# Optimization experiments

Hardware: AMD Instinct MI355X
Metric: run time of the kernel (lower is better)

## Reference

```python
import jax, jax.numpy as jnp
import numpy as np

N_NODES, N_EDGES = 50000, 200000
DN, DE, DG = 256, 256, 128

def setup_inputs() -> dict:
    key = jax.random.key(0)
    ks = jax.random.split(key, 8)
    s = lambda d: 1.0 / np.sqrt(d)
    return {
        "nodes": jax.random.normal(ks[0], (N_NODES, DN), jnp.float32),
        "edges": jax.random.normal(ks[1], (N_EDGES, DE), jnp.float32),
        "globals_": jax.random.normal(ks[2], (DG,), jnp.float32),
        "senders": jax.random.randint(ks[3], (N_EDGES,), 0, N_NODES, jnp.int32),
        "receivers": jax.random.randint(ks[4], (N_EDGES,), 0, N_NODES, jnp.int32),
        "We": jax.random.normal(ks[5], (DE + 2 * DN + DG, DE), jnp.float32) * s(DE + 2 * DN + DG),
        "be": jnp.zeros((DE,), jnp.float32),
        "Wn": jax.random.normal(ks[6], (DE + DN + DG, DN), jnp.float32) * s(DE + DN + DG),
        "bn": jnp.zeros((DN,), jnp.float32),
        "Wg": jax.random.normal(ks[7], (DE + DN + DG, DG), jnp.float32) * s(DE + DN + DG),
        "bg": jnp.zeros((DG,), jnp.float32),
    }

def reference(nodes, edges, globals_, senders, receivers, We, be, Wn, bn, Wg, bg):
    E, N = edges.shape[0], nodes.shape[0]
    # --- edge processor: phi_e([e, v_s, v_r, u]) ---
    edge_in = jnp.concatenate(
        [edges, nodes[senders], nodes[receivers],
         jnp.broadcast_to(globals_, (E, globals_.shape[0]))], axis=-1)  # [E, 896]
    new_edges = jax.nn.relu(edge_in @ We + be)  # [E, DE]
    # --- node processor: phi_v([sum_incoming_e, v, u]) ---
    agg_e = jax.ops.segment_sum(new_edges, receivers, num_segments=N)  # [N, DE]
    node_in = jnp.concatenate(
        [agg_e, nodes, jnp.broadcast_to(globals_, (N, globals_.shape[0]))], axis=-1)
    new_nodes = jax.nn.relu(node_in @ Wn + bn)  # [N, DN]
    # --- global processor: phi_u([sum_e, sum_v, u]) ---
    global_in = jnp.concatenate(
        [new_edges.sum(axis=0), new_nodes.sum(axis=0), globals_], axis=-1)
    new_globals = jax.nn.relu(global_in @ Wg + bg)  # [DG]
    return new_edges, new_nodes, new_globals
```

## Files before the change

kernel.cpp:

```cpp
#include <hip/hip_runtime.h>

#define E_CNT 200000
#define N_CNT 50000

typedef __attribute__((ext_vector_type(8))) unsigned short ushort8;
typedef __attribute__((ext_vector_type(4))) unsigned short us4;
typedef __attribute__((ext_vector_type(4))) float f32x4;
typedef __bf16 bf16x8 __attribute__((ext_vector_type(8)));

static __device__ __forceinline__ unsigned short f2bf(float f) {
  unsigned int u = __builtin_bit_cast(unsigned int, f);
  u += 0x7FFFu + ((u >> 16) & 1u);
  return (unsigned short)(u >> 16);
}
static __device__ __forceinline__ float bf2f(unsigned short u) {
  unsigned int x = ((unsigned int)u) << 16;
  return __builtin_bit_cast(float, x);
}

__global__ void prep_w(const float* __restrict__ W, unsigned short* __restrict__ Bp, int KC) {
  int idx = blockIdx.x * blockDim.x + threadIdx.x;
  int total = KC * 16 * 64;
  if (idx >= total) return;
  int lane = idx & 63;
  int t = idx >> 6;
  int F = t & 15;
  int kc = t >> 4;
  int col = F * 16 + (lane & 15);
  int kb = kc * 32 + (lane >> 4) * 8;
  ushort8 v;
#pragma unroll
  for (int j = 0; j < 8; ++j) v[j] = f2bf(W[(size_t)(kb + j) * 256 + col]);
  *reinterpret_cast<ushort8*>(Bp + (size_t)idx * 8) = v;
}

__global__ void make_cvec(const float* __restrict__ g, const float* __restrict__ We,
                          const float* __restrict__ be, const float* __restrict__ Wn,
                          const float* __restrict__ bn, float* __restrict__ ce,
                          float* __restrict__ cn) {
  int t = threadIdx.x;
  int j = t & 255;
  if (t < 256) {
    float s = be[j];
    for (int k = 0; k < 128; ++k) s += g[k] * We[(size_t)(768 + k) * 256 + j];
    ce[j] = s;
  } else {
    float s = bn[j];
    for (int k = 0; k < 128; ++k) s += g[k] * Wn[(size_t)(512 + k) * 256 + j];
    cn[j] = s;
  }
}

template <int NSTEPS, int MODE>
__global__ __launch_bounds__(512, 2) void gemm_core(
    const float* __restrict__ A0, const float* __restrict__ A1,
    const unsigned short* __restrict__ Bp, const unsigned short* __restrict__ P1,
    const unsigned short* __restrict__ P2, const float* __restrict__ cvec,
    const int* __restrict__ senders, const int* __restrict__ receivers,
    float* __restrict__ outF, unsigned short* __restrict__ outP,
    float* __restrict__ agg, int M) {
  __shared__ unsigned short lds[2][128 * 64];

  const int tid = threadIdx.x;
  const int lane = tid & 63;
  const int wave = tid >> 6;
  const int wm = wave >> 2;
  const int wn = wave & 3;
  const int q = lane >> 4;
  const int lr = lane & 15;
  const int row0 = blockIdx.x * 128;

  const int sr = tid >> 2;
  const int sc = tid & 3;
  int er = row0 + sr;
  if (er > M - 1) er = M - 1;
  const float* sbase[2];
  sbase[0] = A0 + (size_t)er * 256;
  sbase[1] = (MODE == 2) ? (A1 + (size_t)er * 256) : sbase[0];

  const int swz = sr & 7;
  const int wbase = sr * 64;
  const int s0 = ((sc * 2) ^ swz) * 8;
  const int s1 = ((sc * 2 + 1) ^ swz) * 8;

  f32x4 acc[4][4] = {};

  {
    const float4* p4 = reinterpret_cast<const float4*>(sbase[0] + sc * 16);
    float fv[16];
    *reinterpret_cast<float4*>(&fv[0]) = p4[0];
    *reinterpret_cast<float4*>(&fv[4]) = p4[1];
    *reinterpret_cast<float4*>(&fv[8]) = p4[2];
    *reinterpret_cast<float4*>(&fv[12]) = p4[3];
    ushort8 w0, w1;
#pragma unroll
    for (int j = 0; j < 8; ++j) {
      w0[j] = f2bf(fv[j]);
      w1[j] = f2bf(fv[8 + j]);
    }
    *reinterpret_cast<ushort8*>(&lds[0][wbase + s0]) = w0;
    *reinterpret_cast<ushort8*>(&lds[0][wbase + s1]) = w1;
  }
  __syncthreads();

#pragma unroll
  for (int ks = 0; ks < NSTEPS; ++ks) {
    const int cc = ks & 1;

    bf16x8 bfr[2][4];
#pragma unroll
    for (int kk = 0; kk < 2; ++kk) {
      const int kc32 = ks * 2 + kk;
#pragma unroll
      for (int fn = 0; fn < 4; ++fn) {
        const int F = wn * 4 + fn;
        bfr[kk][fn] = __builtin_bit_cast(
            bf16x8, *reinterpret_cast<const ushort8*>(
                        Bp + ((size_t)(kc32 * 16 + F) * 64 + lane) * 8));
      }
    }

    float4 nf0, nf1, nf2, nf3;
    if (ks + 1 < NSTEPS) {
      const float4* p4 = reinterpret_cast<const float4*>(
          sbase[(ks + 1) >> 2] + ((ks + 1) & 3) * 64 + sc * 16);
      nf0 = p4[0];
      nf1 = p4[1];
      nf2 = p4[2];
      nf3 = p4[3];
    }

#pragma unroll
    for (int kk = 0; kk < 2; ++kk) {
      bf16x8 a[4];
#pragma unroll
      for (int fm = 0; fm < 4; ++fm) {
        int r = wm * 64 + fm * 16 + lr;
        int slot = (kk * 4 + q) ^ (r & 7);
        a[fm] = __builtin_bit_cast(
            bf16x8, *reinterpret_cast<const ushort8*>(&lds[cc][r * 64 + slot * 8]));
      }
#pragma unroll
      for (int fm = 0; fm < 4; ++fm)
#pragma unroll
        for (int fn = 0; fn < 4; ++fn)
          acc[fm][fn] = __builtin_amdgcn_mfma_f32_16x16x32_bf16(
              a[fm], bfr[kk][fn], acc[fm][fn], 0, 0, 0);
    }

    if (ks + 1 < NSTEPS) {
      float fv[16];
      *reinterpret_cast<float4*>(&fv[0]) = nf0;
      *reinterpret_cast<float4*>(&fv[4]) = nf1;
      *reinterpret_cast<float4*>(&fv[8]) = nf2;
      *reinterpret_cast<float4*>(&fv[12]) = nf3;
      ushort8 w0, w1;
#pragma unroll
      for (int j = 0; j < 8; ++j) {
        w0[j] = f2bf(fv[j]);
        w1[j] = f2bf(fv[8 + j]);
      }
      *reinterpret_cast<ushort8*>(&lds[cc ^ 1][wbase + s0]) = w0;
      *reinterpret_cast<ushort8*>(&lds[cc ^ 1][wbase + s1]) = w1;
      __syncthreads();
    }
  }

  float bcol[4];
  if (MODE != 0) {
#pragma unroll
    for (int fn = 0; fn < 4; ++fn) bcol[fn] = cvec[wn * 64 + fn * 16 + lr];
  }
#pragma unroll
  for (int fm = 0; fm < 4; ++fm) {
    int rb = row0 + wm * 64 + fm * 16 + q * 4;
#pragma unroll
    for (int i = 0; i < 4; ++i) {
      int gr = rb + i;
      if (gr < M) {
        if (MODE == 0) {
          us4 pv;
#pragma unroll
          for (int fn = 0; fn < 4; ++fn) pv[fn] = f2bf(acc[fm][fn][i]);
          *reinterpret_cast<us4*>(outP + (size_t)gr * 256 + wn * 64 + lr * 4) = pv;
        } else if (MODE == 1) {
          int snd = senders[gr], rcv = receivers[gr];
          us4 ps = *reinterpret_cast<const us4*>(P1 + (size_t)snd * 256 + wn * 64 + lr * 4);
          us4 pr = *reinterpret_cast<const us4*>(P2 + (size_t)rcv * 256 + wn * 64 + lr * 4);
#pragma unroll
          for (int fn = 0; fn < 4; ++fn) {
            int col = wn * 64 + fn * 16 + lr;
            float v = fmaxf(acc[fm][fn][i] + bcol[fn] + bf2f(ps[fn]) + bf2f(pr[fn]), 0.0f);
            __builtin_nontemporal_store(v, &outF[(size_t)gr * 256 + col]);
            atomicAdd(agg + (size_t)rcv * 256 + col, v);
          }
        } else {
#pragma unroll
          for (int fn = 0; fn < 4; ++fn) {
            int col = wn * 64 + fn * 16 + lr;
            outF[(size_t)gr * 256 + col] = fmaxf(acc[fm][fn][i] + bcol[fn], 0.0f);
          }
        }
      }
    }
  }
}

#define CS_PARTS 128
__global__ void colsum_p1(const float* __restrict__ in, float* __restrict__ part, int rows) {
  const int c4 = threadIdx.x & 63;
  const int rg = threadIdx.x >> 6;
  f32x4 s = {0.f, 0.f, 0.f, 0.f};
  for (int r = blockIdx.x * 4 + rg; r < rows; r += CS_PARTS * 4)
    s += *reinterpret_cast<const f32x4*>(in + (size_t)r * 256 + c4 * 4);
  __shared__ f32x4 red[256];
  red[threadIdx.x] = s;
  __syncthreads();
  if (rg == 0) {
    f32x4 r = red[c4] + red[64 + c4] + red[128 + c4] + red[192 + c4];
    *reinterpret_cast<f32x4*>(part + (size_t)blockIdx.x * 256 + c4 * 4) = r;
  }
}

__global__ void colsum_p2(const float* __restrict__ part, float* __restrict__ out) {
  const int c = threadIdx.x;
  float s = 0.f;
  for (int p = 0; p < CS_PARTS; ++p) s += part[(size_t)p * 256 + c];
  out[c] = s;
}

__global__ void global_mlp(const float* __restrict__ esum, const float* __restrict__ nsum,
                           const float* __restrict__ gl, const float* __restrict__ Wg,
                           const float* __restrict__ bg, float* __restrict__ out2) {
  __shared__ float red[512];
  int g = threadIdx.x & 127;
  int kg = threadIdx.x >> 7;
  float acc = 0.f;
  for (int k = kg; k < 640; k += 4) {
    float x = (k < 256) ? esum[k] : (k < 512 ? nsum[k - 256] : gl[k - 512]);
    acc += x * Wg[(size_t)k * 128 + g];
  }
  red[threadIdx.x] = acc;
  __syncthreads();
  if (kg == 0) {
    float r = red[g] + red[128 + g] + red[256 + g] + red[384 + g] + bg[g];
    out2[g] = fmaxf(r, 0.f);
  }
}

extern "C" void kernel_launch(void* const* d_in, const int* in_sizes, int n_in,
                              void* d_out, int out_size, void* d_ws, size_t ws_size,
                              hipStream_t stream) {
  const float* nodes = (const float*)d_in[0];
  const float* edges = (const float*)d_in[1];
  const float* gl = (const float*)d_in[2];
  const int* senders = (const int*)d_in[3];
  const int* receivers = (const int*)d_in[4];
  const float* We = (const float*)d_in[5];
  const float* be = (const float*)d_in[6];
  const float* Wn = (const float*)d_in[7];
  const float* bn = (const float*)d_in[8];
  const float* Wg = (const float*)d_in[9];
  const float* bg = (const float*)d_in[10];

  float* out0 = (float*)d_out;
  float* out1 = out0 + (size_t)E_CNT * 256;
  float* out2 = out1 + (size_t)N_CNT * 256;

  float* agg = out1;

  char* ws = (char*)d_ws;
  size_t o = 0;
  unsigned short* Ps = (unsigned short*)(ws + o);   o += (size_t)N_CNT * 256 * 2;
  unsigned short* Pr = (unsigned short*)(ws + o);   o += (size_t)N_CNT * 256 * 2;
  unsigned short* BpEe = (unsigned short*)(ws + o); o += 131072;
  unsigned short* BpPs = (unsigned short*)(ws + o); o += 131072;
  unsigned short* BpPr = (unsigned short*)(ws + o); o += 131072;
  unsigned short* BpN = (unsigned short*)(ws + o);  o += 262144;
  float* ce = (float*)(ws + o);                     o += 1024;
  float* cn = (float*)(ws + o);                     o += 1024;
  float* esum = (float*)(ws + o);                   o += 1024;
  float* nsum = (float*)(ws + o);                   o += 1024;
  float* partE = (float*)(ws + o);                  o += CS_PARTS * 256 * 4;
  float* partN = (float*)(ws + o);                  o += CS_PARTS * 256 * 4;

  hipMemsetAsync(agg, 0, (size_t)N_CNT * 256 * 4, stream);

  prep_w<<<32, 256, 0, stream>>>(We, BpEe, 8);
  prep_w<<<32, 256, 0, stream>>>(We + 256 * 256, BpPs, 8);
  prep_w<<<32, 256, 0, stream>>>(We + 512 * 256, BpPr, 8);
  prep_w<<<32, 256, 0, stream>>>(Wn, BpN, 8);
  prep_w<<<32, 256, 0, stream>>>(Wn + 256 * 256, BpN + 65536, 8);
  make_cvec<<<1, 512, 0, stream>>>(gl, We, be, Wn, bn, ce, cn);

  gemm_core<4, 0><<<(N_CNT + 127) / 128, 512, 0, stream>>>(
      nodes, nullptr, BpPs, nullptr, nullptr, nullptr, nullptr, nullptr,
      nullptr, Ps, nullptr, N_CNT);
  gemm_core<4, 0><<<(N_CNT + 127) / 128, 512, 0, stream>>>(
      nodes, nullptr, BpPr, nullptr, nullptr, nullptr, nullptr, nullptr,
      nullptr, Pr, nullptr, N_CNT);

  gemm_core<4, 1><<<(E_CNT + 127) / 128, 512, 0, stream>>>(
      edges, nullptr, BpEe, Ps, Pr, ce, senders, receivers, out0, nullptr,
      agg, E_CNT);

  colsum_p1<<<CS_PARTS, 256, 0, stream>>>(agg, partE, N_CNT);
  colsum_p2<<<1, 256, 0, stream>>>(partE, esum);

  gemm_core<8, 2><<<(N_CNT + 127) / 128, 512, 0, stream>>>(
      agg, nodes, BpN, nullptr, nullptr, cn, nullptr, nullptr, out1, nullptr,
      nullptr, N_CNT);

  colsum_p1<<<CS_PARTS, 256, 0, stream>>>(out1, partN, N_CNT);
  colsum_p2<<<1, 256, 0, stream>>>(partN, nsum);

  global_mlp<<<1, 512, 0, stream>>>(esum, nsum, gl, Wg, bg, out2);
}
```

Before: 453.5 us.

## Accumulate edge aggregation with packed bf16 atomics and merge prep launches

The edge-to-node scatter-add now uses packed bf16 global atomics into a bf16 workspace buffer instead of fp32 atomicAdd into the output. This halves atomic traffic and the memset size, and the node GEMM reads the aggregate directly as bf16 without converting it. Because the atomic writes permuted columns, the Wn rows are permuted to match and the edge column sum is un-permuted afterwards. The weight-prep and cvec launches are merged into one kernel, and the two node-projection GEMMs share a single launch. The cost is that the sums are accumulated in bf16, so summing many edges per node loses precision.

```diff
diff --git a/kernel.cpp b/kernel.cpp
--- a/kernel.cpp
+++ b/kernel.cpp
@@ -2,6 +2,7 @@
 
 #define E_CNT 200000
 #define N_CNT 50000
+#define CS_PARTS 128
 
 typedef __attribute__((ext_vector_type(8))) unsigned short ushort8;
 typedef __attribute__((ext_vector_type(4))) unsigned short us4;
@@ -17,11 +18,40 @@
   unsigned int x = ((unsigned int)u) << 16;
   return __builtin_bit_cast(float, x);
 }
-
-__global__ void prep_w(const float* __restrict__ W, unsigned short* __restrict__ Bp, int KC) {
-  int idx = blockIdx.x * blockDim.x + threadIdx.x;
-  int total = KC * 16 * 64;
-  if (idx >= total) return;
+static __device__ __forceinline__ void pk_add_bf16(unsigned short* a, unsigned int v) {
+  asm volatile("global_atomic_pk_add_bf16 %0, %1, off" ::"v"(a), "v"(v) : "memory");
+}
+
+__global__ void prep_all(const float* __restrict__ We, const float* __restrict__ be,
+                         const float* __restrict__ Wn, const float* __restrict__ bn,
+                         const float* __restrict__ g, unsigned short* __restrict__ BpEe,
+                         unsigned short* __restrict__ BpPs, unsigned short* __restrict__ BpPr,
+                         unsigned short* __restrict__ BpN, float* __restrict__ ce,
+                         float* __restrict__ cn) {
+  int bid = blockIdx.x;
+  if (bid >= 160) {
+    int j = threadIdx.x;
+    if (bid == 160) {
+      float s = be[j];
+      for (int k = 0; k < 128; ++k) s += g[k] * We[(size_t)(768 + k) * 256 + j];
+      ce[j] = s;
+    } else {
+      float s = bn[j];
+      for (int k = 0; k < 128; ++k) s += g[k] * Wn[(size_t)(512 + k) * 256 + j];
+      cn[j] = s;
+    }
+    return;
+  }
+  int sub = bid >> 5;
+  const float* W;
+  unsigned short* Bp;
+  bool perm = false;
+  if (sub == 0) { W = We;           Bp = BpEe; }
+  else if (sub == 1) { W = We + 65536;  Bp = BpPs; }
+  else if (sub == 2) { W = We + 131072; Bp = BpPr; }
+  else if (sub == 3) { W = Wn;          Bp = BpN; perm = true; }
+  else { W = Wn + 65536; Bp = BpN + 65536; }
+  int idx = (bid & 31) * 256 + threadIdx.x;
   int lane = idx & 63;
   int t = idx >> 6;
   int F = t & 15;
@@ -30,36 +60,34 @@
   int kb = kc * 32 + (lane >> 4) * 8;
   ushort8 v;
 #pragma unroll
-  for (int j = 0; j < 8; ++j) v[j] = f2bf(W[(size_t)(kb + j) * 256 + col]);
+  for (int j = 0; j < 8; ++j) {
+    int r = kb + j;
+    if (perm) r = (r & ~63) | ((r & 3) << 4) | ((r >> 2) & 15);
+    v[j] = f2bf(W[(size_t)r * 256 + col]);
+  }
   *reinterpret_cast<ushort8*>(Bp + (size_t)idx * 8) = v;
-}
-
-__global__ void make_cvec(const float* __restrict__ g, const float* __restrict__ We,
-                          const float* __restrict__ be, const float* __restrict__ Wn,
-                          const float* __restrict__ bn, float* __restrict__ ce,
-                          float* __restrict__ cn) {
-  int t = threadIdx.x;
-  int j = t & 255;
-  if (t < 256) {
-    float s = be[j];
-    for (int k = 0; k < 128; ++k) s += g[k] * We[(size_t)(768 + k) * 256 + j];
-    ce[j] = s;
-  } else {
-    float s = bn[j];
-    for (int k = 0; k < 128; ++k) s += g[k] * Wn[(size_t)(512 + k) * 256 + j];
-    cn[j] = s;
-  }
 }
 
 template <int NSTEPS, int MODE>
 __global__ __launch_bounds__(512, 2) void gemm_core(
-    const float* __restrict__ A0, const float* __restrict__ A1,
-    const unsigned short* __restrict__ Bp, const unsigned short* __restrict__ P1,
+    const float* __restrict__ A0, const unsigned short* __restrict__ Ab,
+    const float* __restrict__ A1, const unsigned short* __restrict__ Bp,
+    const unsigned short* __restrict__ BpAlt, const unsigned short* __restrict__ P1,
     const unsigned short* __restrict__ P2, const float* __restrict__ cvec,
     const int* __restrict__ senders, const int* __restrict__ receivers,
     float* __restrict__ outF, unsigned short* __restrict__ outP,
-    float* __restrict__ agg, int M) {
+    unsigned short* __restrict__ outPAlt, unsigned short* __restrict__ aggB,
+    int nbHalf, int M) {
   __shared__ unsigned short lds[2][128 * 64];
+
+  int bid = blockIdx.x;
+  const unsigned short* BpL = Bp;
+  unsigned short* outPL = outP;
+  if (MODE == 0 && bid >= nbHalf) {
+    BpL = BpAlt;
+    outPL = outPAlt;
+    bid -= nbHalf;
+  }
 
   const int tid = threadIdx.x;
   const int lane = tid & 63;
@@ -68,15 +96,14 @@
   const int wn = wave & 3;
   const int q = lane >> 4;
   const int lr = lane & 15;
-  const int row0 = blockIdx.x * 128;
+  const int row0 = bid * 128;
 
   const int sr = tid >> 2;
   const int sc = tid & 3;
   int er = row0 + sr;
   if (er > M - 1) er = M - 1;
-  const float* sbase[2];
-  sbase[0] = A0 + (size_t)er * 256;
-  sbase[1] = (MODE == 2) ? (A1 + (size_t)er * 256) : sbase[0];
+  const float* fR = (MODE == 2) ? (A1 + (size_t)er * 256) : (A0 + (size_t)er * 256);
+  const unsigned short* bR = (MODE == 2) ? (Ab + (size_t)er * 256) : nullptr;
 
   const int swz = sr & 7;
   const int wbase = sr * 64;
@@ -85,8 +112,12 @@
 
   f32x4 acc[4][4] = {};
 
-  {
-    const float4* p4 = reinterpret_cast<const float4*>(sbase[0] + sc * 16);
+  if (MODE == 2) {
+    const unsigned short* s = bR + sc * 16;
+    *reinterpret_cast<ushort8*>(&lds[0][wbase + s0]) = *reinterpret_cast<const ushort8*>(s);
+    *reinterpret_cast<ushort8*>(&lds[0][wbase + s1]) = *reinterpret_cast<const ushort8*>(s + 8);
+  } else {
+    const float4* p4 = reinterpret_cast<const float4*>(fR + sc * 16);
     float fv[16];
     *reinterpret_cast<float4*>(&fv[0]) = p4[0];
     *reinterpret_cast<float4*>(&fv[4]) = p4[1];
@@ -116,18 +147,26 @@
         const int F = wn * 4 + fn;
         bfr[kk][fn] = __builtin_bit_cast(
             bf16x8, *reinterpret_cast<const ushort8*>(
-                        Bp + ((size_t)(kc32 * 16 + F) * 64 + lane) * 8));
+                        BpL + ((size_t)(kc32 * 16 + F) * 64 + lane) * 8));
       }
     }
 
     float4 nf0, nf1, nf2, nf3;
+    ushort8 nb0, nb1;
+    const bool nxt_bf = (MODE == 2) && (ks + 1 < 4);
     if (ks + 1 < NSTEPS) {
-      const float4* p4 = reinterpret_cast<const float4*>(
-          sbase[(ks + 1) >> 2] + ((ks + 1) & 3) * 64 + sc * 16);
-      nf0 = p4[0];
-      nf1 = p4[1];
-      nf2 = p4[2];
-      nf3 = p4[3];
+      if (nxt_bf) {
+        const unsigned short* s = bR + (ks + 1) * 64 + sc * 16;
+        nb0 = *reinterpret_cast<const ushort8*>(s);
+        nb1 = *reinterpret_cast<const ushort8*>(s + 8);
+      } else {
+        const float* s = fR + ((MODE == 2) ? (ks + 1 - 4) : (ks + 1)) * 64 + sc * 16;
+        const float4* p4 = reinterpret_cast<const float4*>(s);
+        nf0 = p4[0];
+        nf1 = p4[1];
+        nf2 = p4[2];
+        nf3 = p4[3];
+      }
     }
 
 #pragma unroll
@@ -149,16 +188,21 @@
     }
 
     if (ks + 1 < NSTEPS) {
-      float fv[16];
-      *reinterpret_cast<float4*>(&fv[0]) = nf0;
-      *reinterpret_cast<float4*>(&fv[4]) = nf1;
-      *reinterpret_cast<float4*>(&fv[8]) = nf2;
-      *reinterpret_cast<float4*>(&fv[12]) = nf3;
       ushort8 w0, w1;
-#pragma unroll
-      for (int j = 0; j < 8; ++j) {
-        w0[j] = f2bf(fv[j]);
-        w1[j] = f2bf(fv[8 + j]);
+      if (nxt_bf) {
+        w0 = nb0;
+        w1 = nb1;
+      } else {
+        float fv[16];
+        *reinterpret_cast<float4*>(&fv[0]) = nf0;
+        *reinterpret_cast<float4*>(&fv[4]) = nf1;
+        *reinterpret_cast<float4*>(&fv[8]) = nf2;
+        *reinterpret_cast<float4*>(&fv[12]) = nf3;
+#pragma unroll
+        for (int j = 0; j < 8; ++j) {
+          w0[j] = f2bf(fv[j]);
+          w1[j] = f2bf(fv[8 + j]);
+        }
       }
       *reinterpret_cast<ushort8*>(&lds[cc ^ 1][wbase + s0]) = w0;
       *reinterpret_cast<ushort8*>(&lds[cc ^ 1][wbase + s1]) = w1;
@@ -182,18 +226,24 @@
           us4 pv;
 #pragma unroll
           for (int fn = 0; fn < 4; ++fn) pv[fn] = f2bf(acc[fm][fn][i]);
-          *reinterpret_cast<us4*>(outP + (size_t)gr * 256 + wn * 64 + lr * 4) = pv;
+          *reinterpret_cast<us4*>(outPL + (size_t)gr * 256 + wn * 64 + lr * 4) = pv;
         } else if (MODE == 1) {
           int snd = senders[gr], rcv = receivers[gr];
           us4 ps = *reinterpret_cast<const us4*>(P1 + (size_t)snd * 256 + wn * 64 + lr * 4);
           us4 pr = *reinterpret_cast<const us4*>(P2 + (size_t)rcv * 256 + wn * 64 + lr * 4);
-#pragma unroll
-          for (int fn = 0; fn < 4; ++fn) {
-            int col = wn * 64 + fn * 16 + lr;
-            float v = fmaxf(acc[fm][fn][i] + bcol[fn] + bf2f(ps[fn]) + bf2f(pr[fn]), 0.0f);
-            __builtin_nontemporal_store(v, &outF[(size_t)gr * 256 + col]);
-            atomicAdd(agg + (size_t)rcv * 256 + col, v);
-          }
+          float v[4];
+#pragma unroll
+          for (int fn = 0; fn < 4; ++fn)
+            v[fn] = fmaxf(acc[fm][fn][i] + bcol[fn] + bf2f(ps[fn]) + bf2f(pr[fn]), 0.0f);
+#pragma unroll
+          for (int fn = 0; fn < 4; ++fn)
+            __builtin_nontemporal_store(
+                v[fn], &outF[(size_t)gr * 256 + wn * 64 + fn * 16 + lr]);
+          unsigned int p01 = (unsigned int)f2bf(v[0]) | ((unsigned int)f2bf(v[1]) << 16);
+          unsigned int p23 = (unsigned int)f2bf(v[2]) | ((unsigned int)f2bf(v[3]) << 16);
+          unsigned short* ap = aggB + (size_t)rcv * 256 + wn * 64 + lr * 4;
+          pk_add_bf16(ap, p01);
+          pk_add_bf16(ap + 2, p23);
         } else {
 #pragma unroll
           for (int fn = 0; fn < 4; ++fn) {
@@ -206,7 +256,6 @@
   }
 }
 
-#define CS_PARTS 128
 __global__ void colsum_p1(const float* __restrict__ in, float* __restrict__ part, int rows) {
   const int c4 = threadIdx.x & 63;
   const int rg = threadIdx.x >> 6;
@@ -221,12 +270,36 @@
     *reinterpret_cast<f32x4*>(part + (size_t)blockIdx.x * 256 + c4 * 4) = r;
   }
 }
-
 __global__ void colsum_p2(const float* __restrict__ part, float* __restrict__ out) {
   const int c = threadIdx.x;
   float s = 0.f;
   for (int p = 0; p < CS_PARTS; ++p) s += part[(size_t)p * 256 + c];
   out[c] = s;
+}
+__global__ void colsum_p1b(const unsigned short* __restrict__ in, float* __restrict__ part,
+                           int rows) {
+  const int c4 = threadIdx.x & 63;
+  const int rg = threadIdx.x >> 6;
+  f32x4 s = {0.f, 0.f, 0.f, 0.f};
+  for (int r = blockIdx.x * 4 + rg; r < rows; r += CS_PARTS * 4) {
+    us4 v = *reinterpret_cast<const us4*>(in + (size_t)r * 256 + c4 * 4);
+#pragma unroll
+    for (int j = 0; j < 4; ++j) s[j] += bf2f(v[j]);
+  }
+  __shared__ f32x4 red[256];
+  red[threadIdx.x] = s;
+  __syncthreads();
+  if (rg == 0) {
+    f32x4 r = red[c4] + red[64 + c4] + red[128 + c4] + red[192 + c4];
+    *reinterpret_cast<f32x4*>(part + (size_t)blockIdx.x * 256 + c4 * 4) = r;
+  }
+}
+__global__ void colsum_p2b(const float* __restrict__ part, float* __restrict__ out) {
+  const int s = threadIdx.x;
+  float v = 0.f;
+  for (int p = 0; p < CS_PARTS; ++p) v += part[(size_t)p * 256 + s];
+  int orig = (s & 192) | ((s & 3) << 4) | ((s >> 2) & 15);
+  out[orig] = v;
 }
 
 __global__ void global_mlp(const float* __restrict__ esum, const float* __restrict__ nsum,
@@ -267,12 +340,11 @@
   float* out1 = out0 + (size_t)E_CNT * 256;
   float* out2 = out1 + (size_t)N_CNT * 256;
 
-  float* agg = out1;
-
   char* ws = (char*)d_ws;
   size_t o = 0;
   unsigned short* Ps = (unsigned short*)(ws + o);   o += (size_t)N_CNT * 256 * 2;
   unsigned short* Pr = (unsigned short*)(ws + o);   o += (size_t)N_CNT * 256 * 2;
+  unsigned short* aggB = (unsigned short*)(ws + o); o += (size_t)N_CNT * 256 * 2;
   unsigned short* BpEe = (unsigned short*)(ws + o); o += 131072;
   unsigned short* BpPs = (unsigned short*)(ws + o); o += 131072;
   unsigned short* BpPr = (unsigned short*)(ws + o); o += 131072;
@@ -284,32 +356,25 @@
   float* partE = (float*)(ws + o);                  o += CS_PARTS * 256 * 4;
   float* partN = (float*)(ws + o);                  o += CS_PARTS * 256 * 4;
 
-  hipMemsetAsync(agg, 0, (size_t)N_CNT * 256 * 4, stream);
-
-  prep_w<<<32, 256, 0, stream>>>(We, BpEe, 8);
-  prep_w<<<32, 256, 0, stream>>>(We + 256 * 256, BpPs, 8);
-  prep_w<<<32, 256, 0, stream>>>(We + 512 * 256, BpPr, 8);
-  prep_w<<<32, 256, 0, stream>>>(Wn, BpN, 8);
-  prep_w<<<32, 256, 0, stream>>>(Wn + 256 * 256, BpN + 65536, 8);
-  make_cvec<<<1, 512, 0, stream>>>(gl, We, be, Wn, bn, ce, cn);
-
-  gemm_core<4, 0><<<(N_CNT + 127) / 128, 512, 0, stream>>>(
-      nodes, nullptr, BpPs, nullptr, nullptr, nullptr, nullptr, nullptr,
-      nullptr, Ps, nullptr, N_CNT);
-  gemm_core<4, 0><<<(N_CNT + 127) / 128, 512, 0, stream>>>(
-      nodes, nullptr, BpPr, nullptr, nullptr, nullptr, nullptr, nullptr,
-      nullptr, Pr, nullptr, N_CNT);
+  hipMemsetAsync(aggB, 0, (size_t)N_CNT * 256 * 2, stream);
+
+  prep_all<<<162, 256, 0, stream>>>(We, be, Wn, bn, gl, BpEe, BpPs, BpPr, BpN, ce, cn);
+
+  const int nbN = (N_CNT + 127) / 128;
+  gemm_core<4, 0><<<2 * nbN, 512, 0, stream>>>(
+      nodes, nullptr, nullptr, BpPs, BpPr, nullptr, nullptr, nullptr, nullptr,
+      nullptr, nullptr, Ps, Pr, nullptr, nbN, N_CNT);
 
   gemm_core<4, 1><<<(E_CNT + 127) / 128, 512, 0, stream>>>(
-      edges, nullptr, BpEe, Ps, Pr, ce, senders, receivers, out0, nullptr,
-      agg, E_CNT);
-
-  colsum_p1<<<CS_PARTS, 256, 0, stream>>>(agg, partE, N_CNT);
-  colsum_p2<<<1, 256, 0, stream>>>(partE, esum);
-
-  gemm_core<8, 2><<<(N_CNT + 127) / 128, 512, 0, stream>>>(
-      agg, nodes, BpN, nullptr, nullptr, cn, nullptr, nullptr, out1, nullptr,
-      nullptr, N_CNT);
+      edges, nullptr, nullptr, BpEe, nullptr, Ps, Pr, ce, senders, receivers,
+      out0, nullptr, nullptr, aggB, 1 << 30, E_CNT);
+
+  colsum_p1b<<<CS_PARTS, 256, 0, stream>>>(aggB, partE, N_CNT);
+  colsum_p2b<<<1, 256, 0, stream>>>(partE, esum);
+
+  gemm_core<8, 2><<<nbN, 512, 0, stream>>>(
+      nullptr, aggB, nodes, BpN, nullptr, nullptr, nullptr, cn, nullptr, nullptr,
+      out1, nullptr, nullptr, nullptr, 1 << 30, N_CNT);
 
   colsum_p1<<<CS_PARTS, 256, 0, stream>>>(out1, partN, N_CNT);
   colsum_p2<<<1, 256, 0, stream>>>(partN, nsum);
```

Measured after the change: 449.9 us. About the same (-0.8%).

## Halve GEMM row tile to 64, merge projection GEMMs and prep kernels

Applied to the files above, without the earlier changes.

The row tile of the shared GEMM kernel drops from 128 to 64 rows per block, with half the accumulators, half the LDS, and launch bounds raised to allow up to 8 blocks per CU. The two node-projection GEMMs become one launch that picks its weights and output by block index, and the five weight-packing launches plus the constant-vector kernel become a single prep kernel. The aim is more blocks and better latency hiding across the 256-CU device, plus fewer launches. The cost is that each B fragment loaded from global memory is reused across half as many rows, so weight traffic per output row doubles.

```diff
diff --git a/kernel.cpp b/kernel.cpp
--- a/kernel.cpp
+++ b/kernel.cpp
@@ -2,6 +2,7 @@
 
 #define E_CNT 200000
 #define N_CNT 50000
+#define CS_PARTS 128
 
 typedef __attribute__((ext_vector_type(8))) unsigned short ushort8;
 typedef __attribute__((ext_vector_type(4))) unsigned short us4;
@@ -18,10 +19,35 @@
   return __builtin_bit_cast(float, x);
 }
 
-__global__ void prep_w(const float* __restrict__ W, unsigned short* __restrict__ Bp, int KC) {
-  int idx = blockIdx.x * blockDim.x + threadIdx.x;
-  int total = KC * 16 * 64;
-  if (idx >= total) return;
+__global__ void prep_all(const float* __restrict__ We, const float* __restrict__ be,
+                         const float* __restrict__ Wn, const float* __restrict__ bn,
+                         const float* __restrict__ g, unsigned short* __restrict__ BpEe,
+                         unsigned short* __restrict__ BpPs, unsigned short* __restrict__ BpPr,
+                         unsigned short* __restrict__ BpN, float* __restrict__ ce,
+                         float* __restrict__ cn) {
+  int bid = blockIdx.x;
+  if (bid >= 160) {
+    int j = threadIdx.x;
+    if (bid == 160) {
+      float s = be[j];
+      for (int k = 0; k < 128; ++k) s += g[k] * We[(size_t)(768 + k) * 256 + j];
+      ce[j] = s;
+    } else {
+      float s = bn[j];
+      for (int k = 0; k < 128; ++k) s += g[k] * Wn[(size_t)(512 + k) * 256 + j];
+      cn[j] = s;
+    }
+    return;
+  }
+  int sub = bid >> 5;
+  const float* W;
+  unsigned short* Bp;
+  if (sub == 0)      { W = We;           Bp = BpEe; }
+  else if (sub == 1) { W = We + 65536;   Bp = BpPs; }
+  else if (sub == 2) { W = We + 131072;  Bp = BpPr; }
+  else if (sub == 3) { W = Wn;           Bp = BpN; }
+  else               { W = Wn + 65536;   Bp = BpN + 65536; }
+  int idx = (bid & 31) * 256 + threadIdx.x;
   int lane = idx & 63;
   int t = idx >> 6;
   int F = t & 15;
@@ -34,32 +60,25 @@
   *reinterpret_cast<ushort8*>(Bp + (size_t)idx * 8) = v;
 }
 
-__global__ void make_cvec(const float* __restrict__ g, const float* __restrict__ We,
-                          const float* __restrict__ be, const float* __restrict__ Wn,
-                          const float* __restrict__ bn, float* __restrict__ ce,
-                          float* __restrict__ cn) {
-  int t = threadIdx.x;
-  int j = t & 255;
-  if (t < 256) {
-    float s = be[j];
-    for (int k = 0; k < 128; ++k) s += g[k] * We[(size_t)(768 + k) * 256 + j];
-    ce[j] = s;
-  } else {
-    float s = bn[j];
-    for (int k = 0; k < 128; ++k) s += g[k] * Wn[(size_t)(512 + k) * 256 + j];
-    cn[j] = s;
-  }
-}
-
 template <int NSTEPS, int MODE>
-__global__ __launch_bounds__(512, 2) void gemm_core(
+__global__ __launch_bounds__(512, 8) void gemm_core(
     const float* __restrict__ A0, const float* __restrict__ A1,
-    const unsigned short* __restrict__ Bp, const unsigned short* __restrict__ P1,
-    const unsigned short* __restrict__ P2, const float* __restrict__ cvec,
-    const int* __restrict__ senders, const int* __restrict__ receivers,
-    float* __restrict__ outF, unsigned short* __restrict__ outP,
-    float* __restrict__ agg, int M) {
-  __shared__ unsigned short lds[2][128 * 64];
+    const unsigned short* __restrict__ Bp, const unsigned short* __restrict__ BpAlt,
+    const unsigned short* __restrict__ P1, const unsigned short* __restrict__ P2,
+    const float* __restrict__ cvec, const int* __restrict__ senders,
+    const int* __restrict__ receivers, float* __restrict__ outF,
+    unsigned short* __restrict__ outP, unsigned short* __restrict__ outPAlt,
+    float* __restrict__ agg, int nbHalf, int M) {
+  __shared__ unsigned short lds[2][64 * 64];
+
+  int bid = blockIdx.x;
+  const unsigned short* BpL = Bp;
+  unsigned short* outPL = outP;
+  if (MODE == 0 && bid >= nbHalf) {
+    BpL = BpAlt;
+    outPL = outPAlt;
+    bid -= nbHalf;
+  }
 
   const int tid = threadIdx.x;
   const int lane = tid & 63;
@@ -68,10 +87,10 @@
   const int wn = wave & 3;
   const int q = lane >> 4;
   const int lr = lane & 15;
-  const int row0 = blockIdx.x * 128;
-
-  const int sr = tid >> 2;
-  const int sc = tid & 3;
+  const int row0 = bid * 64;
+
+  const int sr = tid >> 3;
+  const int sc = tid & 7;
   int er = row0 + sr;
   if (er > M - 1) er = M - 1;
   const float* sbase[2];
@@ -80,26 +99,19 @@
 
   const int swz = sr & 7;
   const int wbase = sr * 64;
-  const int s0 = ((sc * 2) ^ swz) * 8;
-  const int s1 = ((sc * 2 + 1) ^ swz) * 8;
-
-  f32x4 acc[4][4] = {};
+  const int s0 = (sc ^ swz) * 8;
+
+  f32x4 acc[2][4] = {};
 
   {
-    const float4* p4 = reinterpret_cast<const float4*>(sbase[0] + sc * 16);
-    float fv[16];
+    const float4* p4 = reinterpret_cast<const float4*>(sbase[0] + sc * 8);
+    float fv[8];
     *reinterpret_cast<float4*>(&fv[0]) = p4[0];
     *reinterpret_cast<float4*>(&fv[4]) = p4[1];
-    *reinterpret_cast<float4*>(&fv[8]) = p4[2];
-    *reinterpret_cast<float4*>(&fv[12]) = p4[3];
-    ushort8 w0, w1;
-#pragma unroll
-    for (int j = 0; j < 8; ++j) {
-      w0[j] = f2bf(fv[j]);
-      w1[j] = f2bf(fv[8 + j]);
-    }
+    ushort8 w0;
+#pragma unroll
+    for (int j = 0; j < 8; ++j) w0[j] = f2bf(fv[j]);
     *reinterpret_cast<ushort8*>(&lds[0][wbase + s0]) = w0;
-    *reinterpret_cast<ushort8*>(&lds[0][wbase + s1]) = w1;
   }
   __syncthreads();
 
@@ -107,61 +119,49 @@
   for (int ks = 0; ks < NSTEPS; ++ks) {
     const int cc = ks & 1;
 
-    bf16x8 bfr[2][4];
+    float4 nf0, nf1;
+    if (ks + 1 < NSTEPS) {
+      const float4* p4 = reinterpret_cast<const float4*>(
+          sbase[(ks + 1) >> 2] + ((ks + 1) & 3) * 64 + sc * 8);
+      nf0 = p4[0];
+      nf1 = p4[1];
+    }
+
 #pragma unroll
     for (int kk = 0; kk < 2; ++kk) {
       const int kc32 = ks * 2 + kk;
+      bf16x8 bfr[4];
 #pragma unroll
       for (int fn = 0; fn < 4; ++fn) {
         const int F = wn * 4 + fn;
-        bfr[kk][fn] = __builtin_bit_cast(
+        bfr[fn] = __builtin_bit_cast(
             bf16x8, *reinterpret_cast<const ushort8*>(
-                        Bp + ((size_t)(kc32 * 16 + F) * 64 + lane) * 8));
+                        BpL + ((size_t)(kc32 * 16 + F) * 64 + lane) * 8));
       }
-    }
-
-    float4 nf0, nf1, nf2, nf3;
-    if (ks + 1 < NSTEPS) {
-      const float4* p4 = reinterpret_cast<const float4*>(
-          sbase[(ks + 1) >> 2] + ((ks + 1) & 3) * 64 + sc * 16);
-      nf0 = p4[0];
-      nf1 = p4[1];
-      nf2 = p4[2];
-      nf3 = p4[3];
-    }
-
-#pragma unroll
-    for (int kk = 0; kk < 2; ++kk) {
-      bf16x8 a[4];
-#pragma unroll
-      for (int fm = 0; fm < 4; ++fm) {
-        int r = wm * 64 + fm * 16 + lr;
+      bf16x8 a[2];
+#pragma unroll
+      for (int fm = 0; fm < 2; ++fm) {
+        int r = wm * 32 + fm * 16 + lr;
         int slot = (kk * 4 + q) ^ (r & 7);
         a[fm] = __builtin_bit_cast(
             bf16x8, *reinterpret_cast<const ushort8*>(&lds[cc][r * 64 + slot * 8]));
       }
 #pragma unroll
-      for (int fm = 0; fm < 4; ++fm)
+      for (int fm = 0; fm < 2; ++fm)
 #pragma unroll
         for (int fn = 0; fn < 4; ++fn)
           acc[fm][fn] = __builtin_amdgcn_mfma_f32_16x16x32_bf16(
-              a[fm], bfr[kk][fn], acc[fm][fn], 0, 0, 0);
+              a[fm], bfr[fn], acc[fm][fn], 0, 0, 0);
     }
 
     if (ks + 1 < NSTEPS) {
-      float fv[16];
+      float fv[8];
       *reinterpret_cast<float4*>(&fv[0]) = nf0;
       *reinterpret_cast<float4*>(&fv[4]) = nf1;
-      *reinterpret_cast<float4*>(&fv[8]) = nf2;
-      *reinterpret_cast<float4*>(&fv[12]) = nf3;
-      ushort8 w0, w1;
-#pragma unroll
-      for (int j = 0; j < 8; ++j) {
-        w0[j] = f2bf(fv[j]);
-        w1[j] = f2bf(fv[8 + j]);
-      }
+      ushort8 w0;
+#pragma unroll
+      for (int j = 0; j < 8; ++j) w0[j] = f2bf(fv[j]);
       *reinterpret_cast<ushort8*>(&lds[cc ^ 1][wbase + s0]) = w0;
-      *reinterpret_cast<ushort8*>(&lds[cc ^ 1][wbase + s1]) = w1;
       __syncthreads();
     }
   }
@@ -172,8 +172,8 @@
     for (int fn = 0; fn < 4; ++fn) bcol[fn] = cvec[wn * 64 + fn * 16 + lr];
   }
 #pragma unroll
-  for (int fm = 0; fm < 4; ++fm) {
-    int rb = row0 + wm * 64 + fm * 16 + q * 4;
+  for (int fm = 0; fm < 2; ++fm) {
+    int rb = row0 + wm * 32 + fm * 16 + q * 4;
 #pragma unroll
     for (int i = 0; i < 4; ++i) {
       int gr = rb + i;
@@ -182,7 +182,7 @@
           us4 pv;
 #pragma unroll
           for (int fn = 0; fn < 4; ++fn) pv[fn] = f2bf(acc[fm][fn][i]);
-          *reinterpret_cast<us4*>(outP + (size_t)gr * 256 + wn * 64 + lr * 4) = pv;
+          *reinterpret_cast<us4*>(outPL + (size_t)gr * 256 + wn * 64 + lr * 4) = pv;
         } else if (MODE == 1) {
           int snd = senders[gr], rcv = receivers[gr];
           us4 ps = *reinterpret_cast<const us4*>(P1 + (size_t)snd * 256 + wn * 64 + lr * 4);
@@ -206,7 +206,6 @@
   }
 }
 
-#define CS_PARTS 128
 __global__ void colsum_p1(const float* __restrict__ in, float* __restrict__ part, int rows) {
   const int c4 = threadIdx.x & 63;
   const int rg = threadIdx.x >> 6;
@@ -286,30 +285,23 @@
 
   hipMemsetAsync(agg, 0, (size_t)N_CNT * 256 * 4, stream);
 
-  prep_w<<<32, 256, 0, stream>>>(We, BpEe, 8);
-  prep_w<<<32, 256, 0, stream>>>(We + 256 * 256, BpPs, 8);
-  prep_w<<<32, 256, 0, stream>>>(We + 512 * 256, BpPr, 8);
-  prep_w<<<32, 256, 0, stream>>>(Wn, BpN, 8);
-  prep_w<<<32, 256, 0, stream>>>(Wn + 256 * 256, BpN + 65536, 8);
-  make_cvec<<<1, 512, 0, stream>>>(gl, We, be, Wn, bn, ce, cn);
-
-  gemm_core<4, 0><<<(N_CNT + 127) / 128, 512, 0, stream>>>(
-      nodes, nullptr, BpPs, nullptr, nullptr, nullptr, nullptr, nullptr,
-      nullptr, Ps, nullptr, N_CNT);
-  gemm_core<4, 0><<<(N_CNT + 127) / 128, 512, 0, stream>>>(
-      nodes, nullptr, BpPr, nullptr, nullptr, nullptr, nullptr, nullptr,
-      nullptr, Pr, nullptr, N_CNT);
-
-  gemm_core<4, 1><<<(E_CNT + 127) / 128, 512, 0, stream>>>(
-      edges, nullptr, BpEe, Ps, Pr, ce, senders, receivers, out0, nullptr,
-      agg, E_CNT);
+  prep_all<<<162, 256, 0, stream>>>(We, be, Wn, bn, gl, BpEe, BpPs, BpPr, BpN, ce, cn);
+
+  const int nbN = (N_CNT + 63) / 64;
+  gemm_core<4, 0><<<2 * nbN, 512, 0, stream>>>(
+      nodes, nullptr, BpPs, BpPr, nullptr, nullptr, nullptr, nullptr, nullptr,
+      nullptr, Ps, Pr, nullptr, nbN, N_CNT);
+
+  gemm_core<4, 1><<<E_CNT / 64, 512, 0, stream>>>(
+      edges, nullptr, BpEe, nullptr, Ps, Pr, ce, senders, receivers, out0,
+      nullptr, nullptr, agg, 1 << 30, E_CNT);
 
   colsum_p1<<<CS_PARTS, 256, 0, stream>>>(agg, partE, N_CNT);
   colsum_p2<<<1, 256, 0, stream>>>(partE, esum);
 
-  gemm_core<8, 2><<<(N_CNT + 127) / 128, 512, 0, stream>>>(
-      agg, nodes, BpN, nullptr, nullptr, cn, nullptr, nullptr, out1, nullptr,
-      nullptr, N_CNT);
+  gemm_core<8, 2><<<nbN, 512, 0, stream>>>(
+      agg, nodes, BpN, nullptr, nullptr, nullptr, cn, nullptr, nullptr, out1,
+      nullptr, nullptr, nullptr, 1 << 30, N_CNT);
 
   colsum_p1<<<CS_PARTS, 256, 0, stream>>>(out1, partN, N_CNT);
   colsum_p2<<<1, 256, 0, stream>>>(partN, nsum);
```

New measurement: 563.3 us. +24.2%, slower.
